# Kernel tuning notes

Measured on AMD Instinct MI355X. Metric: run time of the kernel, lower is better.

The kernel has to match this reference:

```python
import jax, jax.numpy as jnp
import numpy as np

V, H, O = 50257, 1024, 50257
B, T = 32, 512


def setup_inputs() -> dict:
    key = jax.random.key(0)
    ks = jax.random.split(key, 8)
    p = lambda k, shape: 0.02 * jax.random.normal(k, shape, dtype=jnp.float32)
    return {
        "state": jax.random.normal(ks[0], (B, H), dtype=jnp.float32),
        "tokens": jax.random.randint(ks[1], (B, T), 0, V, dtype=jnp.int64),
        "embedding": p(ks[2], (V, H)),
        "ih": p(ks[3], (H, H)),
        "hh": p(ks[4], (H, H)),
        "bias": p(ks[5], (H,)),
        "out_w": p(ks[6], (H, O)),
        "outBias": p(ks[7], (O,)),
    }


def reference(state, tokens, embedding, ih, hh, bias, out_w, outBias):
    # preCompute(): note torch broadcasts (H,H)/(H,) over the LAST axis,
    # i.e. column j is divided by ||hh[j,:]|| * H -- replicated faithfully.
    row_norms = jnp.linalg.norm(hh, axis=1)          # [H]
    scaledHH = hh / (row_norms * H)                  # [H,H]
    embedded = jnp.tanh(embedding) @ ih + bias       # [V,H]

    tokens_t = tokens.T                              # [T,B]

    def step(carry, tok):
        st, loss = carry                             # st: [B,H]
        logits = st @ out_w + outBias                # [B,O]
        logp = jax.nn.log_softmax(logits, axis=-1)
        nll = -jnp.take_along_axis(logp, tok[:, None], axis=1).mean()  # CE, mean over batch
        loss = loss + nll
        e = embedded[tok]                            # [B,H] gather
        # einsum('bi,bj->bi'): state scaled by sum over embedded features
        attn = jax.nn.softmax(st * e.sum(-1, keepdims=True), axis=-1)  # [B,H]
        st = jnp.tanh(st + attn @ scaledHH)
        return (st, loss), None

    (state, loss), _ = jax.lax.scan(step, (state, jnp.zeros((), state.dtype)), tokens_t)
    return state, loss
```

## Files before the change

kernel.cpp:

```cpp
#include <hip/hip_runtime.h>

#define VV 50257
#define HH 1024
#define OO 50257
#define BB 32
#define TT 512
#define NPAD2 50432
#define MROWS 16384
#define NBLK 32
#define KTILES 32

using bf16x8 = __attribute__((ext_vector_type(8))) short;
using f32x4  = __attribute__((ext_vector_type(4))) float;

__device__ __forceinline__ unsigned short f2bf(float x) {
    unsigned u = __float_as_uint(x);
    unsigned r = (u + 0x7FFFu + ((u >> 16) & 1u)) >> 16;
    return (unsigned short)r;
}
__device__ __forceinline__ float bf2f(unsigned short h) {
    return __uint_as_float(((unsigned)h) << 16);
}
__device__ __forceinline__ unsigned hz16(unsigned x) {
    return (x - 0x00010001u) & ~x & 0x80008000u;
}

__device__ __forceinline__ uint4 load_coh16(const void* p) {
    uint4 v;
    asm volatile("global_load_dwordx4 %0, %1, off sc0 sc1" : "=v"(v) : "v"(p));
    return v;
}
__device__ __forceinline__ void store_coh2(void* p, unsigned short s) {
    unsigned v = s;
    asm volatile("global_store_short %0, %1, off sc0 sc1" :: "v"(p), "v"(v) : "memory");
}
__device__ __forceinline__ void gload16(const void* g, void* l) {
    __builtin_amdgcn_global_load_lds((const __attribute__((address_space(1))) unsigned int*)g,
                                     (__attribute__((address_space(3))) unsigned int*)l, 16, 0, 0);
}

__global__ void prep_reduce(const float* __restrict__ ih, const float* __restrict__ hh,
                            const float* __restrict__ bias,
                            float* __restrict__ rs, float* __restrict__ rn, float* __restrict__ bsum) {
    int w = blockIdx.x * 4 + (threadIdx.x >> 6);
    int lane = threadIdx.x & 63;
    if (w < 1024) {
        const float* row = ih + (size_t)w * HH;
        float s = 0.f;
        for (int k = lane; k < HH; k += 64) s += row[k];
        for (int m = 1; m < 64; m <<= 1) s += __shfl_xor(s, m, 64);
        if (lane == 0) rs[w] = s;
    } else if (w < 2048) {
        int r = w - 1024;
        const float* row = hh + (size_t)r * HH;
        float s = 0.f;
        for (int k = lane; k < HH; k += 64) { float x = row[k]; s += x * x; }
        for (int m = 1; m < 64; m <<= 1) s += __shfl_xor(s, m, 64);
        if (lane == 0) rn[r] = sqrtf(s);
    } else if (w == 2048) {
        float s = 0.f;
        for (int k = lane; k < HH; k += 64) s += bias[k];
        for (int m = 1; m < 64; m <<= 1) s += __shfl_xor(s, m, 64);
        if (lane == 0) bsum[0] = s;
    }
}

__global__ void shconv(const float* __restrict__ hh, const float* __restrict__ rn,
                       unsigned short* __restrict__ SHb) {
    int gid = blockIdx.x * 256 + threadIdx.x;
    int slice = gid >> 12, kb = (gid >> 5) & 127, col = gid & 31;
    int j = slice * 32 + col;
    float inv = 1.0f / (rn[j] * 1024.0f);
    unsigned short v[8];
#pragma unroll
    for (int e = 0; e < 8; e++)
        v[e] = f2bf(hh[(size_t)(kb * 8 + e) * HH + j] * inv);
    uint4 pk;
    pk.x = (unsigned)v[0] | ((unsigned)v[1] << 16);
    pk.y = (unsigned)v[2] | ((unsigned)v[3] << 16);
    pk.z = (unsigned)v[4] | ((unsigned)v[5] << 16);
    pk.w = (unsigned)v[6] | ((unsigned)v[7] << 16);
    int gid_sw = (slice << 12) + (kb << 5) + (col ^ (kb & 3));
    *(uint4*)(SHb + (size_t)gid_sw * 8) = pk;
}

__global__ void esum_kernel(const float* __restrict__ emb, const float* __restrict__ rs,
                            const float* __restrict__ bsum, float* __restrict__ esum) {
    __shared__ float rs_l[HH];
    for (int i = threadIdx.x; i < HH; i += 256) rs_l[i] = rs[i];
    __syncthreads();
    int v = blockIdx.x * 4 + (threadIdx.x >> 6);
    if (v >= VV) return;
    int lane = threadIdx.x & 63;
    const float* row = emb + (size_t)v * HH;
    float s = 0.f;
    for (int k = lane; k < HH; k += 64) s += tanhf(row[k]) * rs_l[k];
    for (int m = 1; m < 64; m <<= 1) s += __shfl_xor(s, m, 64);
    if (lane == 0) esum[v] = s + bsum[0];
}

__global__ void esd_k(const int* __restrict__ tokens, const float* __restrict__ esum,
                      float* __restrict__ esd) {
    int idx = blockIdx.x * 256 + threadIdx.x;
    int t = idx >> 5, b = idx & 31;
    esd[idx] = esum[tokens[b * TT + t]];
}

__global__ void wconv(const float* __restrict__ W, unsigned short* __restrict__ Wb) {
    int n = blockIdx.x * 256 + threadIdx.x;
    int kb = blockIdx.y;
    unsigned short v[8];
#pragma unroll
    for (int e = 0; e < 8; e++) {
        float x = (n < OO) ? W[(size_t)(kb * 8 + e) * OO + n] : 0.0f;
        v[e] = f2bf(x);
    }
    uint4 pk;
    pk.x = (unsigned)v[0] | ((unsigned)v[1] << 16);
    pk.y = (unsigned)v[2] | ((unsigned)v[3] << 16);
    pk.z = (unsigned)v[4] | ((unsigned)v[5] << 16);
    pk.w = (unsigned)v[6] | ((unsigned)v[7] << 16);
    *(uint4*)(Wb + ((size_t)kb * NPAD2 + n) * 8) = pk;
}

__global__ void tokd_k(const int* __restrict__ tokens, int* __restrict__ tokd) {
    int r = blockIdx.x * 256 + threadIdx.x;
    int t = r >> 5, b = r & 31;
    tokd[r] = tokens[b * TT + t];
}

__global__ void __launch_bounds__(512) recurrence(
    const float* __restrict__ state_in, const unsigned short* __restrict__ SHb,
    const float* __restrict__ esd, unsigned short* __restrict__ S,
    unsigned short* __restrict__ abuf ,
    unsigned* __restrict__ flags ,
    float* __restrict__ out_state) {
    __shared__ unsigned short Wl[32768];
    __shared__ unsigned short Alds[32768];
    __shared__ f32x4 pacc[4][64];
    __shared__ float den_p[2][8][8];
    const int blk = blockIdx.x;
    const int tid = threadIdx.x;
    const int lane = tid & 63, w = tid >> 6;
    const int wr = (w >> 1) & 1, nt = w & 1, kh = w >> 2;
    const int q = lane >> 4, l16 = lane & 15;

    float st[4];
    const int b0 = wr * 16 + q * 4;
    const int jg = blk * 32 + nt * 16 + l16;
    if (kh == 0) {
#pragma unroll
        for (int r = 0; r < 4; r++) st[r] = state_in[(b0 + r) * HH + jg];
#pragma unroll
        for (int r = 0; r < 4; r++)
            store_coh2(abuf + (size_t)(b0 + r) * HH + jg, f2bf(__expf(st[r] * esd[b0 + r])));
        asm volatile("s_waitcnt vmcnt(0)" ::: "memory");
        if (lane == 0) {
            unsigned one = 1;
            asm volatile("global_store_dword %0, %1, off sc0 sc1"
                         :: "v"(flags + (blk * 4 + w) * 16), "v"(one) : "memory");
        }
    }
    {
        const uint4* src = (const uint4*)(SHb + (size_t)blk * 32768);
        uint4* dst = (uint4*)Wl;
#pragma unroll
        for (int i = 0; i < 8; i++) dst[tid + i * 512] = src[tid + i * 512];
    }

    for (int t = 0; t < TT; t++) {
        f32x4 es4;
        if (kh == 0) {
            int tn = (t < TT - 1) ? t + 1 : TT - 1;
            es4 = *(const f32x4*)&esd[tn * BB + b0];
#pragma unroll
            for (int r = 0; r < 4; r++)
                S[(size_t)(t * BB + b0 + r) * HH + jg] = f2bf(st[r]);
        }
        uint4 v[8];
        {
            const uint4* p0 = (const uint4*)abuf + (size_t)t * 4096 + tid;
            bool ok;
            int spins = 0;
            do {
#pragma unroll
                for (int i = 0; i < 8; i++) v[i] = load_coh16(p0 + i * 512);
                asm volatile("s_waitcnt vmcnt(0)" ::: "memory");
                __builtin_amdgcn_sched_barrier(0);
                unsigned bad = 0;
#pragma unroll
                for (int i = 0; i < 8; i++)
                    bad |= hz16(v[i].x) | hz16(v[i].y) | hz16(v[i].z) | hz16(v[i].w);
                ok = __all(bad == 0);
            } while (!ok && ++spins < 128);
            if (!ok) {
                const unsigned* f0 = flags + (2 * lane) * 16;
                const unsigned* f1 = flags + (2 * lane + 1) * 16;
                unsigned fa, fb;
                do {
                    asm volatile("global_load_dword %0, %2, off sc0 sc1\n\t"
                                 "global_load_dword %1, %3, off sc0 sc1\n\t"
                                 "s_waitcnt vmcnt(0)"
                                 : "=&v"(fa), "=&v"(fb) : "v"(f0), "v"(f1) : "memory");
                } while (!__all((int)(fa >= (unsigned)(t + 1) && fb >= (unsigned)(t + 1))));
#pragma unroll
                for (int i = 0; i < 8; i++) v[i] = load_coh16(p0 + i * 512);
                asm volatile("s_waitcnt vmcnt(0)" ::: "memory");
                __builtin_amdgcn_sched_barrier(0);
            }
        }
        float p[8];
#pragma unroll
        for (int i = 0; i < 8; i++) {
            int c = tid + i * 512;
            int byte = c * 16;
            int row = byte >> 11;
            *(uint4*)((char*)Alds + (byte ^ ((row & 7) << 4))) = v[i];
            float s = 0.f;
            const unsigned short* hp = (const unsigned short*)&v[i];
#pragma unroll
            for (int e = 0; e < 8; e++) s += bf2f(hp[e]);
            p[i] = s;
        }
#pragma unroll
        for (int i = 0; i < 8; i++) {
            float s = p[i];
            for (int m = 1; m < 64; m <<= 1) s += __shfl_xor(s, m, 64);
            p[i] = s;
        }
        if (lane == 0) {
#pragma unroll
            for (int i = 0; i < 8; i++) den_p[t & 1][w][i] = p[i];
        }
        __syncthreads();
        f32x4 acc = {0.f, 0.f, 0.f, 0.f};
#pragma unroll 4
        for (int kt = kh * 16; kt < kh * 16 + 16; kt++) {
            int arow = wr * 16 + l16;
            int abyte = (arow << 11) + kt * 64 + q * 16;
            abyte ^= (arow & 7) << 4;
            bf16x8 af = *(const bf16x8*)((const char*)Alds + abyte);
            int bbyte = ((kt * 4 + q) << 9) + (((nt * 16 + l16) ^ q) << 4);
            bf16x8 bfv = *(const bf16x8*)((const char*)Wl + bbyte);
            acc = __builtin_amdgcn_mfma_f32_16x16x32_bf16(af, bfv, acc, 0, 0, 0);
        }
        const int tile = wr * 2 + nt;
        if (kh == 1) pacc[tile][lane] = acc;
        __syncthreads();
        if (kh == 0) {
            f32x4 other = pacc[tile][lane];
            const bool last = (t == TT - 1);
#pragma unroll
            for (int r = 0; r < 4; r++) {
                float den = den_p[t & 1][2 * r][wr * 4 + q] + den_p[t & 1][2 * r + 1][wr * 4 + q];
                float u = (acc[r] + other[r]) / den;
                float stn = tanhf(st[r] + u);
                st[r] = stn;
                if (!last)
                    store_coh2(abuf + (size_t)(t + 1) * (BB * HH) +
                               (size_t)(b0 + r) * HH + jg, f2bf(__expf(stn * es4[r])));
            }
            if (!last) {
                asm volatile("s_waitcnt vmcnt(0)" ::: "memory");
                if (lane == 0) {
                    unsigned val = (unsigned)(t + 2);
                    asm volatile("global_store_dword %0, %1, off sc0 sc1"
                                 :: "v"(flags + (blk * 4 + w) * 16), "v"(val) : "memory");
                }
            }
        }
    }
    if (kh == 0) {
#pragma unroll
        for (int r = 0; r < 4; r++) out_state[(b0 + r) * HH + jg] = st[r];
    }
}

__global__ void __launch_bounds__(512) gemm_ce(
    const unsigned short* __restrict__ S, const unsigned short* __restrict__ Wb,
    const float* __restrict__ outBias, const int* __restrict__ tokd,
    float* __restrict__ Z, float* __restrict__ lt) {
    __shared__ unsigned short Ab[4][8192];
    __shared__ unsigned short Bb[4][8192];
    const int tid = threadIdx.x;
    const int lane = tid & 63, w = tid >> 6;
    const int wm = w >> 2, wn = w & 3;
    const int lin = blockIdx.x;
    const int id = (lin & 7) * 1576 + (lin >> 3);
    const int grp = id / (197 * 8);
    const int rem = id % (197 * 8);
    const int bx = rem >> 3;
    const int by = (grp << 3) + (rem & 7);
    const int bx256 = bx * 256, by256 = by * 256;

    const int arow = tid >> 2;
    const int rswA = (((tid & 3) ^ (arow & 3)) << 3);
    const unsigned short* AsrcBase = S + (size_t)(by256 + arow) * 1024 + rswA;
    const unsigned short* BsrcBase = Wb + ((size_t)(tid >> 8) * NPAD2 + bx256 + (tid & 255)) * 8;

#define ISSUE_A(kt_) { unsigned short* d = Ab[(kt_) & 3];                         \
    const unsigned short* s0 = AsrcBase + (kt_) * 32;                             \
    gload16(s0, (char*)d + tid * 16);                                             \
    gload16(s0 + 128 * 1024, (char*)d + 8192 + tid * 16); }
#define ISSUE_B(kt_) { unsigned short* d = Bb[(kt_) & 3];                         \
    const unsigned short* s0 = BsrcBase + (size_t)(kt_) * 4 * NPAD2 * 8;          \
    gload16(s0, (char*)d + tid * 16);                                             \
    gload16(s0 + (size_t)2 * NPAD2 * 8, (char*)d + 8192 + tid * 16); }

    f32x4 acc[8][4];
#pragma unroll
    for (int mi = 0; mi < 8; mi++)
#pragma unroll
        for (int ni = 0; ni < 4; ni++) acc[mi][ni] = {0.f, 0.f, 0.f, 0.f};

    ISSUE_A(0); ISSUE_B(0); ISSUE_A(1); ISSUE_B(1);
    asm volatile("s_waitcnt vmcnt(4)" ::: "memory");
    __builtin_amdgcn_s_barrier();

    const int l15 = lane & 15;
    const int slotA = (((lane >> 4) ^ (lane & 3)) << 4);
    const int browA = wm * 128 + l15;
    const int bcolB = ((lane >> 4) << 12) + ((wn * 64 + l15) << 4);

    for (int kt = 0; kt < KTILES; kt++) {
        const char* Abase = (const char*)Ab[kt & 3];
        const char* Bbase = (const char*)Bb[kt & 3];
        bf16x8 af[4], bf[4];
#pragma unroll
        for (int mi = 0; mi < 4; mi++)
            af[mi] = *(const bf16x8*)(Abase + ((browA + mi * 16) << 6) + slotA);
#pragma unroll
        for (int ni = 0; ni < 4; ni++)
            bf[ni] = *(const bf16x8*)(Bbase + bcolB + ni * 256);
        if (kt < KTILES - 2) ISSUE_A(kt + 2);
        __builtin_amdgcn_s_barrier();
        asm volatile("s_waitcnt lgkmcnt(0)" ::: "memory");
        __builtin_amdgcn_sched_barrier(0);
        __builtin_amdgcn_s_setprio(1);
#pragma unroll
        for (int mi = 0; mi < 4; mi++)
#pragma unroll
            for (int ni = 0; ni < 4; ni++)
                acc[mi][ni] = __builtin_amdgcn_mfma_f32_16x16x32_bf16(af[mi], bf[ni], acc[mi][ni], 0, 0, 0);
        __builtin_amdgcn_s_setprio(0);
        __builtin_amdgcn_s_barrier();
#pragma unroll
        for (int mi = 0; mi < 4; mi++)
            af[mi] = *(const bf16x8*)(Abase + ((browA + (mi + 4) * 16) << 6) + slotA);
        if (kt < KTILES - 2) ISSUE_B(kt + 2);
        __builtin_amdgcn_s_barrier();
        asm volatile("s_waitcnt lgkmcnt(0)" ::: "memory");
        __builtin_amdgcn_sched_barrier(0);
        __builtin_amdgcn_s_setprio(1);
#pragma unroll
        for (int mi = 0; mi < 4; mi++)
#pragma unroll
            for (int ni = 0; ni < 4; ni++)
                acc[mi + 4][ni] = __builtin_amdgcn_mfma_f32_16x16x32_bf16(af[mi], bf[ni], acc[mi + 4][ni], 0, 0, 0);
        __builtin_amdgcn_s_setprio(0);
        if (kt < KTILES - 3) {
            asm volatile("s_waitcnt vmcnt(4)" ::: "memory");
        } else if (kt == KTILES - 3) {
            asm volatile("s_waitcnt vmcnt(0)" ::: "memory");
        }
        __builtin_amdgcn_s_barrier();
    }
#undef ISSUE_A
#undef ISSUE_B

    const int colb = bx256 + wn * 64;
    const int rbase = by256 + wm * 128 + ((lane >> 4) << 2);
    float obv[4]; bool okv[4]; int jjv[4];
#pragma unroll
    for (int ni = 0; ni < 4; ni++) {
        jjv[ni] = colb + ni * 16 + l15;
        okv[ni] = jjv[ni] < OO;
        obv[ni] = okv[ni] ? outBias[jjv[ni]] : 0.f;
    }
    float rsum[8][4];
#pragma unroll
    for (int mi = 0; mi < 8; mi++)
#pragma unroll
        for (int r = 0; r < 4; r++) {
            int row = rbase + mi * 16 + r;
            int tk = tokd[row];
            float rssum = 0.f;
#pragma unroll
            for (int ni = 0; ni < 4; ni++) {
                float lg = acc[mi][ni][r] + obv[ni];
                rssum += okv[ni] ? __expf(lg) : 0.f;
                if (okv[ni] && jjv[ni] == tk) lt[row] = lg;
            }
            rsum[mi][r] = rssum;
        }
#pragma unroll
    for (int mi = 0; mi < 8; mi++)
#pragma unroll
        for (int r = 0; r < 4; r++) {
            float s = rsum[mi][r];
            s += __shfl_xor(s, 1, 64); s += __shfl_xor(s, 2, 64);
            s += __shfl_xor(s, 4, 64); s += __shfl_xor(s, 8, 64);
            rsum[mi][r] = s;
        }
    if (l15 == 0) {
#pragma unroll
        for (int mi = 0; mi < 8; mi++)
#pragma unroll
            for (int r = 0; r < 4; r++)
                atomicAdd(&Z[rbase + mi * 16 + r], rsum[mi][r]);
    }
}

__global__ void __launch_bounds__(1024) loss_reduce(const float* __restrict__ Z,
                                                    const float* __restrict__ lt,
                                                    float* __restrict__ out_loss) {
    __shared__ float red[16];
    float s = 0.f;
    for (int r = threadIdx.x; r < MROWS; r += 1024) s += logf(Z[r]) - lt[r];
    for (int m = 1; m < 64; m <<= 1) s += __shfl_xor(s, m, 64);
    if ((threadIdx.x & 63) == 0) red[threadIdx.x >> 6] = s;
    __syncthreads();
    if (threadIdx.x == 0) {
        float tot = 0.f;
        for (int q = 0; q < 16; q++) tot += red[q];
        out_loss[0] = tot / 32.0f;
    }
}

extern "C" void kernel_launch(void* const* d_in, const int* in_sizes, int n_in,
                              void* d_out, int out_size, void* d_ws, size_t ws_size,
                              hipStream_t stream) {
    const float* state  = (const float*)d_in[0];
    const int*   tokens = (const int*)d_in[1];
    const float* emb    = (const float*)d_in[2];
    const float* ih     = (const float*)d_in[3];
    const float* hh     = (const float*)d_in[4];
    const float* bias   = (const float*)d_in[5];
    const float* outw   = (const float*)d_in[6];
    const float* outb   = (const float*)d_in[7];

    char* ws = (char*)d_ws;
    size_t off = 0;
    auto alloc = [&](size_t bytes) { void* p = ws + off; off += (bytes + 255) & ~(size_t)255; return p; };
    unsigned short* Wb  = (unsigned short*)alloc((size_t)128 * NPAD2 * 8 * 2);
    unsigned short* S   = (unsigned short*)alloc((size_t)MROWS * HH * 2);
    unsigned short* abuf= (unsigned short*)alloc((size_t)TT * BB * HH * 2);
    unsigned short* SHb = (unsigned short*)alloc((size_t)131072 * 8 * 2);
    float* esum = (float*)alloc((size_t)VV * 4);
    float* esd  = (float*)alloc((size_t)MROWS * 4);
    float* rs   = (float*)alloc(4096);
    float* rn   = (float*)alloc(4096);
    float* bsum = (float*)alloc(256);
    float* Z    = (float*)alloc((size_t)MROWS * 4);
    float* lt   = (float*)alloc((size_t)MROWS * 4);
    int*   tokd = (int*)alloc((size_t)MROWS * 4);
    unsigned* flags = (unsigned*)alloc(128 * 16 * 4);
    float* out_state = (float*)d_out;
    float* out_loss  = out_state + 32768;

    hipMemsetAsync(Z, 0, (size_t)MROWS * 4, stream);
    hipMemsetAsync(abuf, 0, (size_t)TT * BB * HH * 2, stream);
    hipMemsetAsync(flags, 0, 128 * 16 * 4, stream);
    prep_reduce<<<513, 256, 0, stream>>>(ih, hh, bias, rs, rn, bsum);
    shconv<<<512, 256, 0, stream>>>(hh, rn, SHb);
    esum_kernel<<<12565, 256, 0, stream>>>(emb, rs, bsum, esum);
    esd_k<<<64, 256, 0, stream>>>(tokens, esum, esd);
    wconv<<<dim3(197, 128), 256, 0, stream>>>(outw, Wb);
    tokd_k<<<64, 256, 0, stream>>>(tokens, tokd);
    recurrence<<<NBLK, 512, 0, stream>>>(state, SHb, esd, S, abuf, flags, out_state);
    gemm_ce<<<64 * 197, 512, 0, stream>>>(S, Wb, outb, tokd, Z, lt);
    loss_reduce<<<1, 1024, 0, stream>>>(Z, lt, out_loss);
}
```

Baseline: 4.672 ms.

## Drop flag fallback, pack coherent abuf stores, split MFMA accumulators

```diff
diff --git a/kernel.cpp b/kernel.cpp
--- a/kernel.cpp
+++ b/kernel.cpp
@@ -12,6 +12,7 @@
 
 using bf16x8 = __attribute__((ext_vector_type(8))) short;
 using f32x4  = __attribute__((ext_vector_type(4))) float;
+using u32x4  = __attribute__((ext_vector_type(4))) unsigned int;
 
 __device__ __forceinline__ unsigned short f2bf(float x) {
     unsigned u = __float_as_uint(x);
@@ -29,6 +30,9 @@
     uint4 v;
     asm volatile("global_load_dwordx4 %0, %1, off sc0 sc1" : "=v"(v) : "v"(p));
     return v;
+}
+__device__ __forceinline__ void store_coh16(void* p, u32x4 v) {
+    asm volatile("global_store_dwordx4 %0, %1, off sc0 sc1" :: "v"(p), "v"(v) : "memory");
 }
 __device__ __forceinline__ void store_coh2(void* p, unsigned short s) {
     unsigned v = s;
@@ -133,12 +137,12 @@
     const float* __restrict__ state_in, const unsigned short* __restrict__ SHb,
     const float* __restrict__ esd, unsigned short* __restrict__ S,
     unsigned short* __restrict__ abuf ,
-    unsigned* __restrict__ flags ,
     float* __restrict__ out_state) {
     __shared__ unsigned short Wl[32768];
     __shared__ unsigned short Alds[32768];
     __shared__ f32x4 pacc[4][64];
     __shared__ float den_p[2][8][8];
+    __shared__ unsigned short stg[4][16][16];
     const int blk = blockIdx.x;
     const int tid = threadIdx.x;
     const int lane = tid & 63, w = tid >> 6;
@@ -154,12 +158,6 @@
 #pragma unroll
         for (int r = 0; r < 4; r++)
             store_coh2(abuf + (size_t)(b0 + r) * HH + jg, f2bf(__expf(st[r] * esd[b0 + r])));
-        asm volatile("s_waitcnt vmcnt(0)" ::: "memory");
-        if (lane == 0) {
-            unsigned one = 1;
-            asm volatile("global_store_dword %0, %1, off sc0 sc1"
-                         :: "v"(flags + (blk * 4 + w) * 16), "v"(one) : "memory");
-        }
     }
     {
         const uint4* src = (const uint4*)(SHb + (size_t)blk * 32768);
@@ -181,7 +179,6 @@
         {
             const uint4* p0 = (const uint4*)abuf + (size_t)t * 4096 + tid;
             bool ok;
-            int spins = 0;
             do {
 #pragma unroll
                 for (int i = 0; i < 8; i++) v[i] = load_coh16(p0 + i * 512);
@@ -192,22 +189,8 @@
                 for (int i = 0; i < 8; i++)
                     bad |= hz16(v[i].x) | hz16(v[i].y) | hz16(v[i].z) | hz16(v[i].w);
                 ok = __all(bad == 0);
-            } while (!ok && ++spins < 128);
-            if (!ok) {
-                const unsigned* f0 = flags + (2 * lane) * 16;
-                const unsigned* f1 = flags + (2 * lane + 1) * 16;
-                unsigned fa, fb;
-                do {
-                    asm volatile("global_load_dword %0, %2, off sc0 sc1\n\t"
-                                 "global_load_dword %1, %3, off sc0 sc1\n\t"
-                                 "s_waitcnt vmcnt(0)"
-                                 : "=&v"(fa), "=&v"(fb) : "v"(f0), "v"(f1) : "memory");
-                } while (!__all((int)(fa >= (unsigned)(t + 1) && fb >= (unsigned)(t + 1))));
-#pragma unroll
-                for (int i = 0; i < 8; i++) v[i] = load_coh16(p0 + i * 512);
-                asm volatile("s_waitcnt vmcnt(0)" ::: "memory");
-                __builtin_amdgcn_sched_barrier(0);
-            }
+                if (!ok) __builtin_amdgcn_s_sleep(1);
+            } while (!ok);
         }
         float p[8];
 #pragma unroll
@@ -233,41 +216,56 @@
             for (int i = 0; i < 8; i++) den_p[t & 1][w][i] = p[i];
         }
         __syncthreads();
-        f32x4 acc = {0.f, 0.f, 0.f, 0.f};
-#pragma unroll 4
-        for (int kt = kh * 16; kt < kh * 16 + 16; kt++) {
-            int arow = wr * 16 + l16;
+        f32x4 acc0 = {0.f, 0.f, 0.f, 0.f}, acc1 = {0.f, 0.f, 0.f, 0.f};
+        const int arow = wr * 16 + l16;
+#pragma unroll
+        for (int kk = 0; kk < 8; kk++) {
+            int kt = kh * 16 + kk;
             int abyte = (arow << 11) + kt * 64 + q * 16;
             abyte ^= (arow & 7) << 4;
             bf16x8 af = *(const bf16x8*)((const char*)Alds + abyte);
             int bbyte = ((kt * 4 + q) << 9) + (((nt * 16 + l16) ^ q) << 4);
             bf16x8 bfv = *(const bf16x8*)((const char*)Wl + bbyte);
-            acc = __builtin_amdgcn_mfma_f32_16x16x32_bf16(af, bfv, acc, 0, 0, 0);
-        }
+            acc0 = __builtin_amdgcn_mfma_f32_16x16x32_bf16(af, bfv, acc0, 0, 0, 0);
+            int kt2 = kt + 8;
+            int abyte2 = (arow << 11) + kt2 * 64 + q * 16;
+            abyte2 ^= (arow & 7) << 4;
+            bf16x8 af2 = *(const bf16x8*)((const char*)Alds + abyte2);
+            int bbyte2 = ((kt2 * 4 + q) << 9) + (((nt * 16 + l16) ^ q) << 4);
+            bf16x8 bfv2 = *(const bf16x8*)((const char*)Wl + bbyte2);
+            acc1 = __builtin_amdgcn_mfma_f32_16x16x32_bf16(af2, bfv2, acc1, 0, 0, 0);
+        }
+        f32x4 acc = acc0 + acc1;
         const int tile = wr * 2 + nt;
         if (kh == 1) pacc[tile][lane] = acc;
         __syncthreads();
         if (kh == 0) {
+            __builtin_amdgcn_s_setprio(1);
             f32x4 other = pacc[tile][lane];
             const bool last = (t == TT - 1);
+            unsigned short av[4];
 #pragma unroll
             for (int r = 0; r < 4; r++) {
                 float den = den_p[t & 1][2 * r][wr * 4 + q] + den_p[t & 1][2 * r + 1][wr * 4 + q];
                 float u = (acc[r] + other[r]) / den;
                 float stn = tanhf(st[r] + u);
                 st[r] = stn;
-                if (!last)
-                    store_coh2(abuf + (size_t)(t + 1) * (BB * HH) +
-                               (size_t)(b0 + r) * HH + jg, f2bf(__expf(stn * es4[r])));
+                av[r] = f2bf(__expf(stn * es4[r]));
             }
             if (!last) {
-                asm volatile("s_waitcnt vmcnt(0)" ::: "memory");
-                if (lane == 0) {
-                    unsigned val = (unsigned)(t + 2);
-                    asm volatile("global_store_dword %0, %1, off sc0 sc1"
-                                 :: "v"(flags + (blk * 4 + w) * 16), "v"(val) : "memory");
+#pragma unroll
+                for (int r = 0; r < 4; r++) stg[w][q * 4 + r][l16] = av[r];
+                asm volatile("s_waitcnt lgkmcnt(0)" ::: "memory");
+                __builtin_amdgcn_sched_barrier(0);
+                if (lane < 32) {
+                    int rr = lane & 15, h = lane >> 4;
+                    u32x4 pk = *(const u32x4*)&stg[w][rr][h * 8];
+                    unsigned short* dst = abuf + (size_t)(t + 1) * (BB * HH) +
+                                          (size_t)(wr * 16 + rr) * HH + blk * 32 + nt * 16 + h * 8;
+                    store_coh16(dst, pk);
                 }
             }
+            __builtin_amdgcn_s_setprio(0);
         }
     }
     if (kh == 0) {
@@ -454,20 +452,18 @@
     float* Z    = (float*)alloc((size_t)MROWS * 4);
     float* lt   = (float*)alloc((size_t)MROWS * 4);
     int*   tokd = (int*)alloc((size_t)MROWS * 4);
-    unsigned* flags = (unsigned*)alloc(128 * 16 * 4);
     float* out_state = (float*)d_out;
     float* out_loss  = out_state + 32768;
 
     hipMemsetAsync(Z, 0, (size_t)MROWS * 4, stream);
     hipMemsetAsync(abuf, 0, (size_t)TT * BB * HH * 2, stream);
-    hipMemsetAsync(flags, 0, 128 * 16 * 4, stream);
     prep_reduce<<<513, 256, 0, stream>>>(ih, hh, bias, rs, rn, bsum);
     shconv<<<512, 256, 0, stream>>>(hh, rn, SHb);
     esum_kernel<<<12565, 256, 0, stream>>>(emb, rs, bsum, esum);
     esd_k<<<64, 256, 0, stream>>>(tokens, esum, esd);
     wconv<<<dim3(197, 128), 256, 0, stream>>>(outw, Wb);
     tokd_k<<<64, 256, 0, stream>>>(tokens, tokd);
-    recurrence<<<NBLK, 512, 0, stream>>>(state, SHb, esd, S, abuf, flags, out_state);
+    recurrence<<<NBLK, 512, 0, stream>>>(state, SHb, esd, S, abuf, out_state);
     gemm_ce<<<64 * 197, 512, 0, stream>>>(S, Wb, outb, tokd, Z, lt);
     loss_reduce<<<1, 1024, 0, stream>>>(Z, lt, out_loss);
 }
```

Measured after the change: 4.730 ms. About the same (+1.3%).
